# Kernel optimization log

Hardware: AMD Instinct MI355X
Metric: run time of the kernel (lower is better)

Reference implementation:

```python
import jax, jax.numpy as jnp
import numpy as np


def _edge_conv(h, edge_index, W, b, n_sp):
    # torch_geometric EdgeConv: message = nn(cat[x_i, x_j - x_i]), aggr='max' at target i
    src, dst = edge_index[0], edge_index[1]
    x_i = h[dst]            # [E, d] target features
    x_j = h[src]            # [E, d] source features
    m = jnp.concatenate([x_i, x_j - x_i], axis=-1)  # [E, 2d]
    m = jax.nn.relu(m @ W + b)                       # [E, d_out]
    out = jax.ops.segment_max(m, dst, num_segments=n_sp)
    return jnp.where(jnp.isfinite(out), out, 0.0)    # nodes w/o in-edges -> 0


def setup_inputs() -> dict:
    key = jax.random.key(0)
    ks = jax.random.split(key, 12)
    H, W, C = 512, 512, 128
    OC, NC = 128, 16
    NSP, E = 16384, 262144
    x = jax.random.normal(ks[0], (H, W, C), jnp.float32)
    edge_index = jax.random.randint(ks[1], (2, E), 0, NSP, jnp.int32)
    seg = jax.random.randint(ks[2], (H * W,), 0, NSP, jnp.int32)

    def lin(k, fan_in, shape):
        s = 1.0 / np.sqrt(fan_in)
        return jax.random.uniform(k, shape, jnp.float32, -s, s)

    W1 = lin(ks[3], 2 * C, (2 * C, OC)); b1 = lin(ks[4], 2 * C, (OC,))
    W2 = lin(ks[5], 2 * OC, (2 * OC, OC)); b2 = lin(ks[6], 2 * OC, (OC,))
    Wc = lin(ks[7], OC * 9, (OC, OC, 3, 3)); bc = lin(ks[8], OC * 9, (OC,))
    Wl = lin(ks[9], OC, (OC, NC)); bl = lin(ks[10], OC, (NC,))
    return dict(x=x, edge_index=edge_index, seg=seg, n_sp=NSP,
                W1=W1, b1=b1, W2=W2, b2=b2, Wc=Wc, bc=bc, Wl=Wl, bl=bl)


def reference(x, edge_index, seg, n_sp, W1, b1, W2, b2, Wc, bc, Wl, bl):
    h, w, c = x.shape
    x_flat = x.reshape(h * w, c)
    # Q_Hat_T @ x : mean-pool pixels into superpixels
    counts = jax.ops.segment_sum(jnp.ones((h * w,), x.dtype), seg, num_segments=n_sp)
    sp = jax.ops.segment_sum(x_flat, seg, num_segments=n_sp)
    sp = sp / jnp.maximum(counts, 1.0)[:, None]      # [n_sp, c]
    H1 = _edge_conv(sp, edge_index, W1, b1, n_sp)
    H2 = _edge_conv(H1, edge_index, W2, b2, n_sp)
    H3 = _edge_conv(H2, edge_index, W2, b2, n_sp)    # forward reuses GNN2 (faithful)
    H4 = H1 + H2 + H3
    # Qmatrix @ H4 : unpool superpixel features back to pixels
    img = H4[seg].reshape(1, h, w, -1).transpose(0, 3, 1, 2)  # [1, OC, h, w]
    img = jax.lax.conv_general_dilated(
        img, Wc, window_strides=(1, 1), padding=((1, 1), (1, 1)),
        dimension_numbers=('NCHW', 'OIHW', 'NCHW')) + bc[None, :, None, None]
    out = img[0].transpose(1, 2, 0).reshape(h * w, -1)
    return out @ Wl + bl
```

## Files before the change

kernel.cpp:

```cpp
#include <hip/hip_runtime.h>
#include <hip/hip_bf16.h>
#include <cstdint>

#define HW_PIX 262144
#define NSP    16384
#define NE     262144
#define CH     128
#define IMG    512

typedef __attribute__((ext_vector_type(8))) short bf16x8;
typedef __attribute__((ext_vector_type(4))) float f32x4;

__device__ __forceinline__ float b2f(unsigned short u) {
    union { float f; uint32_t i; } v; v.i = ((uint32_t)u) << 16; return v.f;
}
__device__ __forceinline__ unsigned short f2b(float f) {
    union { float f; uint32_t i; } v; v.f = f;
    uint32_t r = (v.i + 0x7FFFu + ((v.i >> 16) & 1u)) >> 16;
    return (unsigned short)r;
}

__global__ void prep_all_kernel(const float* __restrict__ W1, const float* __restrict__ b1,
                                const float* __restrict__ W2, const float* __restrict__ b2,
                                const float* __restrict__ Wc, const float* __restrict__ Wl,
                                const float* __restrict__ bc, const float* __restrict__ bl,
                                unsigned short* __restrict__ Bp1, float* __restrict__ bias1,
                                unsigned short* __restrict__ Bp2, float* __restrict__ bias2,
                                unsigned short* __restrict__ BpM, float* __restrict__ bout,
                                int* __restrict__ cpix, int* __restrict__ cedge) {
    int b = blockIdx.x;
    if (b < 256) {
        const float* W  = (b < 128) ? W1 : W2;
        const float* bb = (b < 128) ? b1 : b2;
        unsigned short* Bp = (b < 128) ? Bp1 : Bp2;
        float* bias = (b < 128) ? bias1 : bias2;
        int i = (b & 127) * 256 + threadIdx.x;
        int j = i & 7, c = (i >> 3) & 15, g = (i >> 7) & 15, t = i >> 11;
        int k = g * 8 + j, n = t * 16 + c;
        float v;
        if (n < 128) v = W[k * 128 + n] - W[(k + 128) * 128 + n];
        else         v = W[(k + 128) * 128 + (n - 128)];
        Bp[i] = f2b(v);
        if (i < 256) bias[i] = (i < 128) ? bb[i] : 0.f;
    } else if (b < 328) {
        int i = (b - 256) * 256 + threadIdx.x;
        if (i < 18432) {
            int j = i & 7, c = (i >> 3) & 15, g = (i >> 7) & 15, t = i >> 11;
            int k = g * 8 + j;
            float s = 0.f;
            for (int o = 0; o < 128; ++o)
                s += Wc[(size_t)(o * 128 + k) * 9 + t] * Wl[o * 16 + c];
            BpM[i] = f2b(s);
        }
        if (i < 16) {
            float s = bl[i];
            for (int cc = 0; cc < 128; ++cc) s += bc[cc] * Wl[cc * 16 + i];
            bout[i] = s;
        }
    } else {
        int i = (b - 328) * 256 + threadIdx.x;
        if (i < NSP) cpix[i] = 0; else cedge[i - NSP] = 0;
    }
}

__global__ void hist_both_kernel(const int* __restrict__ seg, const int* __restrict__ ei,
                                 int* __restrict__ cpix, int* __restrict__ cedge) {
    int b = blockIdx.x;
    if (b < HW_PIX / 256) {
        int i = b * 256 + threadIdx.x;
        atomicAdd(&cpix[seg[i]], 1);
    } else {
        int e = (b - HW_PIX / 256) * 256 + threadIdx.x;
        atomicAdd(&cedge[ei[NE + e]], 1);
    }
}

__global__ __launch_bounds__(1024) void scan_kernel(const int* __restrict__ cpix, int* __restrict__ opix, int* __restrict__ curpix,
                                                    const int* __restrict__ cedge, int* __restrict__ oedge, int* __restrict__ curedge) {
    const int* cnt = (blockIdx.x == 0) ? cpix : cedge;
    int* offs      = (blockIdx.x == 0) ? opix : oedge;
    int* cur       = (blockIdx.x == 0) ? curpix : curedge;
    __shared__ int tsum[1024];
    int tid = threadIdx.x;
    int loc[16];
    int s = 0;
    #pragma unroll
    for (int q = 0; q < 4; ++q) {
        int4 v = ((const int4*)cnt)[tid * 4 + q];
        loc[q*4+0] = v.x; loc[q*4+1] = v.y; loc[q*4+2] = v.z; loc[q*4+3] = v.w;
    }
    #pragma unroll
    for (int i = 0; i < 16; ++i) { int t = loc[i]; loc[i] = s; s += t; }
    tsum[tid] = s;
    __syncthreads();
    for (int d = 1; d < 1024; d <<= 1) {
        int v = (tid >= d) ? tsum[tid - d] : 0;
        __syncthreads();
        tsum[tid] += v;
        __syncthreads();
    }
    int prefix = tid ? tsum[tid - 1] : 0;
    int base = tid * 16;
    #pragma unroll
    for (int i = 0; i < 16; ++i) { int o = prefix + loc[i]; offs[base + i] = o; cur[base + i] = o; }
    if (tid == 1023) offs[16384] = tsum[1023];
}

__global__ void scatter_both_kernel(const int* __restrict__ seg, const int* __restrict__ ei,
                                    int* __restrict__ cur_pix, int* __restrict__ cur_edge,
                                    int* __restrict__ sorted_pix, int* __restrict__ sorted_src) {
    int b = blockIdx.x;
    if (b < HW_PIX / 256) {
        int p = b * 256 + threadIdx.x;
        int s = seg[p];
        int pos = atomicAdd(&cur_pix[s], 1);
        sorted_pix[pos] = p;
    } else {
        int e = (b - HW_PIX / 256) * 256 + threadIdx.x;
        int d = ei[NE + e];
        int pos = atomicAdd(&cur_edge[d], 1);
        sorted_src[pos] = ei[e];
    }
}

__global__ __launch_bounds__(128) void pool_kernel(const float* __restrict__ x, const int* __restrict__ offs,
                                                   const int* __restrict__ spix, unsigned short* __restrict__ sp) {
    int n = blockIdx.x;
    int c = threadIdx.x;
    int i0 = offs[n], i1 = offs[n + 1];
    float a0 = 0.f, a1 = 0.f, a2 = 0.f, a3 = 0.f, a4 = 0.f, a5 = 0.f, a6 = 0.f, a7 = 0.f;
    int i = i0;
    for (; i + 8 <= i1; i += 8) {
        int p0 = spix[i],   p1 = spix[i+1], p2 = spix[i+2], p3 = spix[i+3];
        int p4 = spix[i+4], p5 = spix[i+5], p6 = spix[i+6], p7 = spix[i+7];
        a0 += x[(size_t)p0 * CH + c];
        a1 += x[(size_t)p1 * CH + c];
        a2 += x[(size_t)p2 * CH + c];
        a3 += x[(size_t)p3 * CH + c];
        a4 += x[(size_t)p4 * CH + c];
        a5 += x[(size_t)p5 * CH + c];
        a6 += x[(size_t)p6 * CH + c];
        a7 += x[(size_t)p7 * CH + c];
    }
    for (; i + 4 <= i1; i += 4) {
        int p0 = spix[i], p1 = spix[i+1], p2 = spix[i+2], p3 = spix[i+3];
        a0 += x[(size_t)p0 * CH + c];
        a1 += x[(size_t)p1 * CH + c];
        a2 += x[(size_t)p2 * CH + c];
        a3 += x[(size_t)p3 * CH + c];
    }
    for (; i < i1; ++i) a0 += x[(size_t)spix[i] * CH + c];
    float acc = ((a0 + a1) + (a2 + a3)) + ((a4 + a5) + (a6 + a7));
    sp[(size_t)n * CH + c] = f2b(acc / fmaxf((float)(i1 - i0), 1.f));
}

__global__ __launch_bounds__(256) void gemm_pq_kernel(const unsigned short* __restrict__ A,
                                                      const unsigned short* __restrict__ Bp,
                                                      const float* __restrict__ bias,
                                                      unsigned short* __restrict__ Pb,
                                                      unsigned short* __restrict__ Qb) {
    int tid = threadIdx.x, wid = tid >> 6, lane = tid & 63;
    int lo = lane & 15, kg = lane >> 4;
    int row = blockIdx.x * 64 + wid * 16 + lo;
    const bf16x8* Arow = (const bf16x8*)(A + (size_t)row * 128);
    int gt0 = blockIdx.y * 4;
    f32x4 acc0 = {0,0,0,0}, acc1 = {0,0,0,0}, acc2 = {0,0,0,0}, acc3 = {0,0,0,0};
    #pragma unroll
    for (int s = 0; s < 4; ++s) {
        bf16x8 a = Arow[s * 4 + kg];
        const bf16x8* B0 = (const bf16x8*)Bp + ((gt0 * 16 + s * 4 + kg) * 16 + lo);
        acc0 = __builtin_amdgcn_mfma_f32_16x16x32_bf16(a, B0[0],   acc0, 0, 0, 0);
        acc1 = __builtin_amdgcn_mfma_f32_16x16x32_bf16(a, B0[256], acc1, 0, 0, 0);
        acc2 = __builtin_amdgcn_mfma_f32_16x16x32_bf16(a, B0[512], acc2, 0, 0, 0);
        acc3 = __builtin_amdgcn_mfma_f32_16x16x32_bf16(a, B0[768], acc3, 0, 0, 0);
    }
    int rowbase = blockIdx.x * 64 + wid * 16 + kg * 4;
    #pragma unroll
    for (int t = 0; t < 4; ++t) {
        f32x4 acc = (t == 0) ? acc0 : (t == 1) ? acc1 : (t == 2) ? acc2 : acc3;
        int gt = gt0 + t;
        int gcol = gt * 16 + lo;
        float bv = bias[gcol];
        unsigned short* dst = (gt < 8) ? Pb : Qb;
        int col = (gt < 8) ? gcol : (gcol - 128);
        #pragma unroll
        for (int r = 0; r < 4; ++r)
            dst[(size_t)(rowbase + r) * 128 + col] = f2b(acc[r] + bv);
    }
}

__global__ __launch_bounds__(256) void gemm_tl_kernel(const unsigned short* __restrict__ H1,
                                                      const unsigned short* __restrict__ H2,
                                                      const unsigned short* __restrict__ H3,
                                                      const unsigned short* __restrict__ BpM,
                                                      float* __restrict__ TL) {
    int tid = threadIdx.x, wid = tid >> 6, lane = tid & 63;
    int lo = lane & 15, kg = lane >> 4;
    int row = blockIdx.x * 64 + wid * 16 + lo;
    int gt0 = blockIdx.y * 4;
    f32x4 acc0 = {0,0,0,0}, acc1 = {0,0,0,0}, acc2 = {0,0,0,0}, acc3 = {0,0,0,0};
    #pragma unroll
    for (int s = 0; s < 4; ++s) {
        int ci = row * 16 + s * 4 + kg;
        bf16x8 a1 = ((const bf16x8*)H1)[ci];
        bf16x8 a2 = ((const bf16x8*)H2)[ci];
        bf16x8 a3 = ((const bf16x8*)H3)[ci];
        bf16x8 a;
        #pragma unroll
        for (int j = 0; j < 8; ++j)
            a[j] = (short)f2b(b2f((unsigned short)a1[j]) + b2f((unsigned short)a2[j]) + b2f((unsigned short)a3[j]));
        const bf16x8* B0 = (const bf16x8*)BpM + ((gt0 * 16 + s * 4 + kg) * 16 + lo);
        if (gt0 + 0 < 9) acc0 = __builtin_amdgcn_mfma_f32_16x16x32_bf16(a, B0[0],   acc0, 0, 0, 0);
        if (gt0 + 1 < 9) acc1 = __builtin_amdgcn_mfma_f32_16x16x32_bf16(a, B0[256], acc1, 0, 0, 0);
        if (gt0 + 2 < 9) acc2 = __builtin_amdgcn_mfma_f32_16x16x32_bf16(a, B0[512], acc2, 0, 0, 0);
        if (gt0 + 3 < 9) acc3 = __builtin_amdgcn_mfma_f32_16x16x32_bf16(a, B0[768], acc3, 0, 0, 0);
    }
    int rowbase = blockIdx.x * 64 + wid * 16 + kg * 4;
    #pragma unroll
    for (int t = 0; t < 4; ++t) {
        if (gt0 + t < 9) {
            f32x4 acc = (t == 0) ? acc0 : (t == 1) ? acc1 : (t == 2) ? acc2 : acc3;
            int gcol = (gt0 + t) * 16 + lo;
            #pragma unroll
            for (int r = 0; r < 4; ++r)
                TL[(size_t)(rowbase + r) * 144 + gcol] = acc[r];
        }
    }
}

__global__ __launch_bounds__(256) void edge_max_kernel(const unsigned short* __restrict__ Pb,
                                                       const unsigned short* __restrict__ Qb,
                                                       const int* __restrict__ offs,
                                                       const int* __restrict__ src,
                                                       unsigned short* __restrict__ H) {
    int n = blockIdx.x * 4 + (threadIdx.x >> 6);
    int lane = threadIdx.x & 63;
    int c = lane * 2;
    int i0 = offs[n], i1 = offs[n + 1];
    const unsigned short* Q = Qb + c;
    float m0 = -3.0e38f, m1 = -3.0e38f;
    int i = i0;
    for (; i + 8 <= i1; i += 8) {
        int s0 = src[i],   s1 = src[i+1], s2 = src[i+2], s3 = src[i+3];
        int s4 = src[i+4], s5 = src[i+5], s6 = src[i+6], s7 = src[i+7];
        uint32_t q0 = *(const uint32_t*)(Q + (size_t)s0 * 128);
        uint32_t q1 = *(const uint32_t*)(Q + (size_t)s1 * 128);
        uint32_t q2 = *(const uint32_t*)(Q + (size_t)s2 * 128);
        uint32_t q3 = *(const uint32_t*)(Q + (size_t)s3 * 128);
        uint32_t q4 = *(const uint32_t*)(Q + (size_t)s4 * 128);
        uint32_t q5 = *(const uint32_t*)(Q + (size_t)s5 * 128);
        uint32_t q6 = *(const uint32_t*)(Q + (size_t)s6 * 128);
        uint32_t q7 = *(const uint32_t*)(Q + (size_t)s7 * 128);
        float l0 = fmaxf(fmaxf(b2f((unsigned short)(q0 & 0xffff)), b2f((unsigned short)(q1 & 0xffff))),
                         fmaxf(b2f((unsigned short)(q2 & 0xffff)), b2f((unsigned short)(q3 & 0xffff))));
        float l1 = fmaxf(fmaxf(b2f((unsigned short)(q4 & 0xffff)), b2f((unsigned short)(q5 & 0xffff))),
                         fmaxf(b2f((unsigned short)(q6 & 0xffff)), b2f((unsigned short)(q7 & 0xffff))));
        float h0 = fmaxf(fmaxf(b2f((unsigned short)(q0 >> 16)), b2f((unsigned short)(q1 >> 16))),
                         fmaxf(b2f((unsigned short)(q2 >> 16)), b2f((unsigned short)(q3 >> 16))));
        float h1 = fmaxf(fmaxf(b2f((unsigned short)(q4 >> 16)), b2f((unsigned short)(q5 >> 16))),
                         fmaxf(b2f((unsigned short)(q6 >> 16)), b2f((unsigned short)(q7 >> 16))));
        m0 = fmaxf(m0, fmaxf(l0, l1));
        m1 = fmaxf(m1, fmaxf(h0, h1));
    }
    for (; i + 4 <= i1; i += 4) {
        int s0 = src[i], s1 = src[i+1], s2 = src[i+2], s3 = src[i+3];
        uint32_t q0 = *(const uint32_t*)(Q + (size_t)s0 * 128);
        uint32_t q1 = *(const uint32_t*)(Q + (size_t)s1 * 128);
        uint32_t q2 = *(const uint32_t*)(Q + (size_t)s2 * 128);
        uint32_t q3 = *(const uint32_t*)(Q + (size_t)s3 * 128);
        m0 = fmaxf(m0, fmaxf(fmaxf(b2f((unsigned short)(q0 & 0xffff)), b2f((unsigned short)(q1 & 0xffff))),
                             fmaxf(b2f((unsigned short)(q2 & 0xffff)), b2f((unsigned short)(q3 & 0xffff)))));
        m1 = fmaxf(m1, fmaxf(fmaxf(b2f((unsigned short)(q0 >> 16)), b2f((unsigned short)(q1 >> 16))),
                             fmaxf(b2f((unsigned short)(q2 >> 16)), b2f((unsigned short)(q3 >> 16)))));
    }
    for (; i < i1; ++i) {
        int s0 = src[i];
        uint32_t q0 = *(const uint32_t*)(Q + (size_t)s0 * 128);
        m0 = fmaxf(m0, b2f((unsigned short)(q0 & 0xffff)));
        m1 = fmaxf(m1, b2f((unsigned short)(q0 >> 16)));
    }
    uint32_t pv = *(const uint32_t*)(Pb + (size_t)n * 128 + c);
    float a0 = fmaxf(0.f, b2f((unsigned short)(pv & 0xffff)) + m0);
    float a1 = fmaxf(0.f, b2f((unsigned short)(pv >> 16)) + m1);
    *(uint32_t*)(H + (size_t)n * 128 + c) = (uint32_t)f2b(a0) | ((uint32_t)f2b(a1) << 16);
}

__global__ __launch_bounds__(256) void conv_out_kernel(const int* __restrict__ seg, const float* __restrict__ TL,
                                                       const float* __restrict__ bout, float* __restrict__ out) {
    int p = blockIdx.x * 256 + threadIdx.x;
    int y = p >> 9, x = p & 511;
    f32x4 a0 = *(const f32x4*)(bout);
    f32x4 a1 = *(const f32x4*)(bout + 4);
    f32x4 a2 = *(const f32x4*)(bout + 8);
    f32x4 a3 = *(const f32x4*)(bout + 12);
    #pragma unroll
    for (int ky = 0; ky < 3; ++ky) {
        int ny = y + ky - 1;
        if ((unsigned)ny >= (unsigned)IMG) continue;
        #pragma unroll
        for (int kx = 0; kx < 3; ++kx) {
            int nx = x + kx - 1;
            if ((unsigned)nx >= (unsigned)IMG) continue;
            const float* t = TL + (size_t)seg[ny * IMG + nx] * 144 + (ky * 3 + kx) * 16;
            a0 += *(const f32x4*)(t);
            a1 += *(const f32x4*)(t + 4);
            a2 += *(const f32x4*)(t + 8);
            a3 += *(const f32x4*)(t + 12);
        }
    }
    float* o = out + (size_t)p * 16;
    *(f32x4*)(o)      = a0;
    *(f32x4*)(o + 4)  = a1;
    *(f32x4*)(o + 8)  = a2;
    *(f32x4*)(o + 12) = a3;
}

extern "C" void kernel_launch(void* const* d_in, const int* in_sizes, int n_in,
                              void* d_out, int out_size, void* d_ws, size_t ws_size,
                              hipStream_t stream) {
    const float* x   = (const float*)d_in[0];
    const int*   ei  = (const int*)d_in[1];
    const int*   seg = (const int*)d_in[2];
    const float* W1  = (const float*)d_in[4];
    const float* b1  = (const float*)d_in[5];
    const float* W2  = (const float*)d_in[6];
    const float* b2  = (const float*)d_in[7];
    const float* Wc  = (const float*)d_in[8];
    const float* bc  = (const float*)d_in[9];
    const float* Wl  = (const float*)d_in[10];
    const float* bl  = (const float*)d_in[11];
    float* out = (float*)d_out;

    char* w = (char*)d_ws;
    auto alloc = [&](size_t bytes) -> void* {
        void* r = (void*)w;
        w += (bytes + 255) & ~(size_t)255;
        return r;
    };
    int* counts_pix  = (int*)alloc(16384 * 4);
    int* offs_pix    = (int*)alloc(16385 * 4);
    int* cur_pix     = (int*)alloc(16384 * 4);
    int* sorted_pix  = (int*)alloc((size_t)HW_PIX * 4);
    int* counts_edge = (int*)alloc(16384 * 4);
    int* offs_edge   = (int*)alloc(16385 * 4);
    int* cur_edge    = (int*)alloc(16384 * 4);
    int* sorted_src  = (int*)alloc((size_t)NE * 4);
    unsigned short* sp  = (unsigned short*)alloc((size_t)NSP * 128 * 2);
    unsigned short* Pb  = (unsigned short*)alloc((size_t)NSP * 128 * 2);
    unsigned short* Qb  = (unsigned short*)alloc((size_t)NSP * 128 * 2);
    unsigned short* H1  = (unsigned short*)alloc((size_t)NSP * 128 * 2);
    unsigned short* H2  = (unsigned short*)alloc((size_t)NSP * 128 * 2);
    unsigned short* H3  = (unsigned short*)alloc((size_t)NSP * 128 * 2);
    float* TL = (float*)alloc((size_t)NSP * 144 * 4);
    unsigned short* Bp1 = (unsigned short*)alloc(32768 * 2);
    unsigned short* Bp2 = (unsigned short*)alloc(32768 * 2);
    unsigned short* BpM = (unsigned short*)alloc(18432 * 2);
    float* bias1 = (float*)alloc(256 * 4);
    float* bias2 = (float*)alloc(256 * 4);
    float* boutb = (float*)alloc(16 * 4);

    prep_all_kernel<<<456, 256, 0, stream>>>(W1, b1, W2, b2, Wc, Wl, bc, bl,
                                             Bp1, bias1, Bp2, bias2, BpM, boutb,
                                             counts_pix, counts_edge);
    hist_both_kernel<<<2048, 256, 0, stream>>>(seg, ei, counts_pix, counts_edge);
    scan_kernel<<<2, 1024, 0, stream>>>(counts_pix, offs_pix, cur_pix, counts_edge, offs_edge, cur_edge);
    scatter_both_kernel<<<2048, 256, 0, stream>>>(seg, ei, cur_pix, cur_edge, sorted_pix, sorted_src);

    pool_kernel<<<NSP, 128, 0, stream>>>(x, offs_pix, sorted_pix, sp);

    dim3 gPQ(NSP / 64, 4);
    dim3 gTL(NSP / 64, 3);

    gemm_pq_kernel<<<gPQ, 256, 0, stream>>>(sp, Bp1, bias1, Pb, Qb);
    edge_max_kernel<<<NSP / 4, 256, 0, stream>>>(Pb, Qb, offs_edge, sorted_src, H1);
    gemm_pq_kernel<<<gPQ, 256, 0, stream>>>(H1, Bp2, bias2, Pb, Qb);
    edge_max_kernel<<<NSP / 4, 256, 0, stream>>>(Pb, Qb, offs_edge, sorted_src, H2);
    gemm_pq_kernel<<<gPQ, 256, 0, stream>>>(H2, Bp2, bias2, Pb, Qb);
    edge_max_kernel<<<NSP / 4, 256, 0, stream>>>(Pb, Qb, offs_edge, sorted_src, H3);

    gemm_tl_kernel<<<gTL, 256, 0, stream>>>(H1, H2, H3, BpM, TL);

    conv_out_kernel<<<HW_PIX / 256, 256, 0, stream>>>(seg, TL, boutb, out);
}
```

Baseline: 204.4 us.

## Reuse A fragments across column groups, add nontemporal loads/stores, pack pool blocks

The PQ and TL GEMMs now have each block cover more output column tiles, so A rows are loaded once and reused instead of being reloaded by extra grid.y blocks. In the TL kernel this also avoids repeating the H1+H2+H3 sum in each block. Pool now handles two superpixels per 256-thread block and reads x with nontemporal loads, and the conv output is written with nontemporal stores to limit cache pollution. In exchange there are fewer blocks in flight for the small GEMMs and more register pressure.

```diff
diff --git a/kernel.cpp b/kernel.cpp
--- a/kernel.cpp
+++ b/kernel.cpp
@@ -123,33 +123,33 @@
     }
 }
 
-__global__ __launch_bounds__(128) void pool_kernel(const float* __restrict__ x, const int* __restrict__ offs,
+__global__ __launch_bounds__(256) void pool_kernel(const float* __restrict__ x, const int* __restrict__ offs,
                                                    const int* __restrict__ spix, unsigned short* __restrict__ sp) {
-    int n = blockIdx.x;
-    int c = threadIdx.x;
+    int n = blockIdx.x * 2 + (threadIdx.x >> 7);
+    int c = threadIdx.x & 127;
     int i0 = offs[n], i1 = offs[n + 1];
     float a0 = 0.f, a1 = 0.f, a2 = 0.f, a3 = 0.f, a4 = 0.f, a5 = 0.f, a6 = 0.f, a7 = 0.f;
     int i = i0;
     for (; i + 8 <= i1; i += 8) {
         int p0 = spix[i],   p1 = spix[i+1], p2 = spix[i+2], p3 = spix[i+3];
         int p4 = spix[i+4], p5 = spix[i+5], p6 = spix[i+6], p7 = spix[i+7];
-        a0 += x[(size_t)p0 * CH + c];
-        a1 += x[(size_t)p1 * CH + c];
-        a2 += x[(size_t)p2 * CH + c];
-        a3 += x[(size_t)p3 * CH + c];
-        a4 += x[(size_t)p4 * CH + c];
-        a5 += x[(size_t)p5 * CH + c];
-        a6 += x[(size_t)p6 * CH + c];
-        a7 += x[(size_t)p7 * CH + c];
+        a0 += __builtin_nontemporal_load(x + (size_t)p0 * CH + c);
+        a1 += __builtin_nontemporal_load(x + (size_t)p1 * CH + c);
+        a2 += __builtin_nontemporal_load(x + (size_t)p2 * CH + c);
+        a3 += __builtin_nontemporal_load(x + (size_t)p3 * CH + c);
+        a4 += __builtin_nontemporal_load(x + (size_t)p4 * CH + c);
+        a5 += __builtin_nontemporal_load(x + (size_t)p5 * CH + c);
+        a6 += __builtin_nontemporal_load(x + (size_t)p6 * CH + c);
+        a7 += __builtin_nontemporal_load(x + (size_t)p7 * CH + c);
     }
     for (; i + 4 <= i1; i += 4) {
         int p0 = spix[i], p1 = spix[i+1], p2 = spix[i+2], p3 = spix[i+3];
-        a0 += x[(size_t)p0 * CH + c];
-        a1 += x[(size_t)p1 * CH + c];
-        a2 += x[(size_t)p2 * CH + c];
-        a3 += x[(size_t)p3 * CH + c];
-    }
-    for (; i < i1; ++i) a0 += x[(size_t)spix[i] * CH + c];
+        a0 += __builtin_nontemporal_load(x + (size_t)p0 * CH + c);
+        a1 += __builtin_nontemporal_load(x + (size_t)p1 * CH + c);
+        a2 += __builtin_nontemporal_load(x + (size_t)p2 * CH + c);
+        a3 += __builtin_nontemporal_load(x + (size_t)p3 * CH + c);
+    }
+    for (; i < i1; ++i) a0 += __builtin_nontemporal_load(x + (size_t)spix[i] * CH + c);
     float acc = ((a0 + a1) + (a2 + a3)) + ((a4 + a5) + (a6 + a7));
     sp[(size_t)n * CH + c] = f2b(acc / fmaxf((float)(i1 - i0), 1.f));
 }
@@ -163,29 +163,33 @@
     int lo = lane & 15, kg = lane >> 4;
     int row = blockIdx.x * 64 + wid * 16 + lo;
     const bf16x8* Arow = (const bf16x8*)(A + (size_t)row * 128);
-    int gt0 = blockIdx.y * 4;
-    f32x4 acc0 = {0,0,0,0}, acc1 = {0,0,0,0}, acc2 = {0,0,0,0}, acc3 = {0,0,0,0};
-    #pragma unroll
-    for (int s = 0; s < 4; ++s) {
-        bf16x8 a = Arow[s * 4 + kg];
-        const bf16x8* B0 = (const bf16x8*)Bp + ((gt0 * 16 + s * 4 + kg) * 16 + lo);
-        acc0 = __builtin_amdgcn_mfma_f32_16x16x32_bf16(a, B0[0],   acc0, 0, 0, 0);
-        acc1 = __builtin_amdgcn_mfma_f32_16x16x32_bf16(a, B0[256], acc1, 0, 0, 0);
-        acc2 = __builtin_amdgcn_mfma_f32_16x16x32_bf16(a, B0[512], acc2, 0, 0, 0);
-        acc3 = __builtin_amdgcn_mfma_f32_16x16x32_bf16(a, B0[768], acc3, 0, 0, 0);
-    }
+    bf16x8 av0 = Arow[kg], av1 = Arow[4 + kg], av2 = Arow[8 + kg], av3 = Arow[12 + kg];
     int rowbase = blockIdx.x * 64 + wid * 16 + kg * 4;
     #pragma unroll
-    for (int t = 0; t < 4; ++t) {
-        f32x4 acc = (t == 0) ? acc0 : (t == 1) ? acc1 : (t == 2) ? acc2 : acc3;
-        int gt = gt0 + t;
-        int gcol = gt * 16 + lo;
-        float bv = bias[gcol];
-        unsigned short* dst = (gt < 8) ? Pb : Qb;
-        int col = (gt < 8) ? gcol : (gcol - 128);
-        #pragma unroll
-        for (int r = 0; r < 4; ++r)
-            dst[(size_t)(rowbase + r) * 128 + col] = f2b(acc[r] + bv);
+    for (int half = 0; half < 2; ++half) {
+        int gt0 = (blockIdx.y * 2 + half) * 4;
+        f32x4 acc0 = {0,0,0,0}, acc1 = {0,0,0,0}, acc2 = {0,0,0,0}, acc3 = {0,0,0,0};
+        #pragma unroll
+        for (int s = 0; s < 4; ++s) {
+            bf16x8 a = (s == 0) ? av0 : (s == 1) ? av1 : (s == 2) ? av2 : av3;
+            const bf16x8* B0 = (const bf16x8*)Bp + ((gt0 * 16 + s * 4 + kg) * 16 + lo);
+            acc0 = __builtin_amdgcn_mfma_f32_16x16x32_bf16(a, B0[0],   acc0, 0, 0, 0);
+            acc1 = __builtin_amdgcn_mfma_f32_16x16x32_bf16(a, B0[256], acc1, 0, 0, 0);
+            acc2 = __builtin_amdgcn_mfma_f32_16x16x32_bf16(a, B0[512], acc2, 0, 0, 0);
+            acc3 = __builtin_amdgcn_mfma_f32_16x16x32_bf16(a, B0[768], acc3, 0, 0, 0);
+        }
+        #pragma unroll
+        for (int t = 0; t < 4; ++t) {
+            f32x4 acc = (t == 0) ? acc0 : (t == 1) ? acc1 : (t == 2) ? acc2 : acc3;
+            int gt = gt0 + t;
+            int gcol = gt * 16 + lo;
+            float bv = bias[gcol];
+            unsigned short* dst = (gt < 8) ? Pb : Qb;
+            int col = (gt < 8) ? gcol : (gcol - 128);
+            #pragma unroll
+            for (int r = 0; r < 4; ++r)
+                dst[(size_t)(rowbase + r) * 128 + col] = f2b(acc[r] + bv);
+        }
     }
 }
 
@@ -197,8 +201,7 @@
     int tid = threadIdx.x, wid = tid >> 6, lane = tid & 63;
     int lo = lane & 15, kg = lane >> 4;
     int row = blockIdx.x * 64 + wid * 16 + lo;
-    int gt0 = blockIdx.y * 4;
-    f32x4 acc0 = {0,0,0,0}, acc1 = {0,0,0,0}, acc2 = {0,0,0,0}, acc3 = {0,0,0,0};
+    bf16x8 af[4];
     #pragma unroll
     for (int s = 0; s < 4; ++s) {
         int ci = row * 16 + s * 4 + kg;
@@ -209,21 +212,30 @@
         #pragma unroll
         for (int j = 0; j < 8; ++j)
             a[j] = (short)f2b(b2f((unsigned short)a1[j]) + b2f((unsigned short)a2[j]) + b2f((unsigned short)a3[j]));
-        const bf16x8* B0 = (const bf16x8*)BpM + ((gt0 * 16 + s * 4 + kg) * 16 + lo);
-        if (gt0 + 0 < 9) acc0 = __builtin_amdgcn_mfma_f32_16x16x32_bf16(a, B0[0],   acc0, 0, 0, 0);
-        if (gt0 + 1 < 9) acc1 = __builtin_amdgcn_mfma_f32_16x16x32_bf16(a, B0[256], acc1, 0, 0, 0);
-        if (gt0 + 2 < 9) acc2 = __builtin_amdgcn_mfma_f32_16x16x32_bf16(a, B0[512], acc2, 0, 0, 0);
-        if (gt0 + 3 < 9) acc3 = __builtin_amdgcn_mfma_f32_16x16x32_bf16(a, B0[768], acc3, 0, 0, 0);
+        af[s] = a;
     }
     int rowbase = blockIdx.x * 64 + wid * 16 + kg * 4;
-    #pragma unroll
-    for (int t = 0; t < 4; ++t) {
-        if (gt0 + t < 9) {
-            f32x4 acc = (t == 0) ? acc0 : (t == 1) ? acc1 : (t == 2) ? acc2 : acc3;
-            int gcol = (gt0 + t) * 16 + lo;
-            #pragma unroll
-            for (int r = 0; r < 4; ++r)
-                TL[(size_t)(rowbase + r) * 144 + gcol] = acc[r];
+    int ng = (blockIdx.y == 0) ? 2 : 1;
+    for (int g = 0; g < ng; ++g) {
+        int gt0 = (blockIdx.y == 0) ? g * 4 : 8;
+        f32x4 acc0 = {0,0,0,0}, acc1 = {0,0,0,0}, acc2 = {0,0,0,0}, acc3 = {0,0,0,0};
+        #pragma unroll
+        for (int s = 0; s < 4; ++s) {
+            const bf16x8* B0 = (const bf16x8*)BpM + ((gt0 * 16 + s * 4 + kg) * 16 + lo);
+            if (gt0 + 0 < 9) acc0 = __builtin_amdgcn_mfma_f32_16x16x32_bf16(af[s], B0[0],   acc0, 0, 0, 0);
+            if (gt0 + 1 < 9) acc1 = __builtin_amdgcn_mfma_f32_16x16x32_bf16(af[s], B0[256], acc1, 0, 0, 0);
+            if (gt0 + 2 < 9) acc2 = __builtin_amdgcn_mfma_f32_16x16x32_bf16(af[s], B0[512], acc2, 0, 0, 0);
+            if (gt0 + 3 < 9) acc3 = __builtin_amdgcn_mfma_f32_16x16x32_bf16(af[s], B0[768], acc3, 0, 0, 0);
+        }
+        #pragma unroll
+        for (int t = 0; t < 4; ++t) {
+            if (gt0 + t < 9) {
+                f32x4 acc = (t == 0) ? acc0 : (t == 1) ? acc1 : (t == 2) ? acc2 : acc3;
+                int gcol = (gt0 + t) * 16 + lo;
+                #pragma unroll
+                for (int r = 0; r < 4; ++r)
+                    TL[(size_t)(rowbase + r) * 144 + gcol] = acc[r];
+            }
         }
     }
 }
@@ -309,10 +321,10 @@
         }
     }
     float* o = out + (size_t)p * 16;
-    *(f32x4*)(o)      = a0;
-    *(f32x4*)(o + 4)  = a1;
-    *(f32x4*)(o + 8)  = a2;
-    *(f32x4*)(o + 12) = a3;
+    __builtin_nontemporal_store(a0, (f32x4*)(o));
+    __builtin_nontemporal_store(a1, (f32x4*)(o + 4));
+    __builtin_nontemporal_store(a2, (f32x4*)(o + 8));
+    __builtin_nontemporal_store(a3, (f32x4*)(o + 12));
 }
 
 extern "C" void kernel_launch(void* const* d_in, const int* in_sizes, int n_in,
@@ -366,10 +378,10 @@
     scan_kernel<<<2, 1024, 0, stream>>>(counts_pix, offs_pix, cur_pix, counts_edge, offs_edge, cur_edge);
     scatter_both_kernel<<<2048, 256, 0, stream>>>(seg, ei, cur_pix, cur_edge, sorted_pix, sorted_src);
 
-    pool_kernel<<<NSP, 128, 0, stream>>>(x, offs_pix, sorted_pix, sp);
-
-    dim3 gPQ(NSP / 64, 4);
-    dim3 gTL(NSP / 64, 3);
+    pool_kernel<<<NSP / 2, 256, 0, stream>>>(x, offs_pix, sorted_pix, sp);
+
+    dim3 gPQ(NSP / 64, 2);
+    dim3 gTL(NSP / 64, 2);
 
     gemm_pq_kernel<<<gPQ, 256, 0, stream>>>(sp, Bp1, bias1, Pb, Qb);
     edge_max_kernel<<<NSP / 4, 256, 0, stream>>>(Pb, Qb, offs_edge, sorted_src, H1);
```

After: 213.0 us (median of 2 runs). +4.2%, slower.
